# Kernel optimization log

Measured on AMD Instinct MI355X. Metric: run time of the kernel, lower is better.

## Reference

```python
import jax, jax.numpy as jnp
import numpy as np

EPS = 1e-06
H_BW = 0.5  # bandwidth h


def setup_inputs() -> dict:
    key = jax.random.key(0)
    k1, k2 = jax.random.split(key)
    N, C, H, W = 8, 256, 64, 64
    x = jax.random.normal(k1, (N, C, H, W), dtype=jnp.float32)
    y = jax.random.normal(k2, (N, C, H, W), dtype=jnp.float32)
    return {"x": x, "y": y}


def reference(x, y):
    N, C, _H, _W = x.shape
    # mean over W, H, then batch -> per-channel mean, shape (1, C, 1, 1)
    y_mu = y.mean(axis=3).mean(axis=2).mean(axis=0).reshape(1, C, 1, 1)
    x_c = x - y_mu
    y_c = y - y_mu
    # L2-normalize over channel dim (matches torch.norm without eps)
    x_n = x_c / jnp.linalg.norm(x_c, axis=1, keepdims=True)
    y_n = y_c / jnp.linalg.norm(y_c, axis=1, keepdims=True)
    x_n = x_n.reshape(N, C, -1)  # (N, C, HW)
    y_n = y_n.reshape(N, C, -1)
    # cosine similarity: (N, HW, HW)
    cosine_sim = jnp.einsum('nci,ncj->nij', x_n, y_n)
    d = 1.0 - cosine_sim
    d_min = jnp.min(d, axis=2, keepdims=True)
    d_tilde = d / (d_min + EPS)
    w = jnp.exp((1.0 - d_tilde) / H_BW)
    ccx_ij = w / jnp.sum(w, axis=2, keepdims=True)
    ccx = jnp.mean(jnp.max(ccx_ij, axis=1), axis=1)  # (N,)
    return jnp.mean(-jnp.log(ccx + EPS))
```

## Files before the change

### kernel.cpp

```cpp
#include <hip/hip_runtime.h>
#include <hip/hip_bf16.h>

#define HW 4096
#define CC 256
#define NBATCH 8
#define EPSF 1e-6f
#define SCL1 0x7F7F7F7F

typedef __attribute__((ext_vector_type(4))) float floatx4;
typedef __attribute__((ext_vector_type(8))) int intx8;
typedef long long llong;

#define GLDS(g, l) __builtin_amdgcn_global_load_lds( \
    (const __attribute__((address_space(1))) void*)(const void*)(g), \
    (__attribute__((address_space(3))) void*)(void*)(l), 16, 0, 0)

__device__ __forceinline__ unsigned fkey(float f){
    unsigned u = __float_as_uint(f);
    return (u & 0x80000000u) ? ~u : (u | 0x80000000u);
}
__device__ __forceinline__ float fdec(unsigned k){
    unsigned u = (k & 0x80000000u) ? (k ^ 0x80000000u) : ~k;
    return __uint_as_float(u);
}
__device__ __forceinline__ unsigned short f2bf(float f){
    unsigned u = __float_as_uint(f);
    u += 0x7FFFu + ((u >> 16) & 1);
    return (unsigned short)(u >> 16);
}

__global__ __launch_bounds__(256) void kmean(const float* __restrict__ y,
                                             float* __restrict__ ymu){
    const int c = blockIdx.x;
    const int t = threadIdx.x;
    float s = 0.f;
    for(int n = 0; n < NBATCH; n++){
        const float4* p = reinterpret_cast<const float4*>(y + ((size_t)n*CC + c)*HW);
        #pragma unroll
        for(int i = 0; i < 4; i++){
            float4 v = p[i*256 + t];
            s += (v.x + v.y) + (v.z + v.w);
        }
    }
    __shared__ float red[256];
    red[t] = s; __syncthreads();
    for(int off = 128; off > 0; off >>= 1){
        if(t < off) red[t] += red[t+off];
        __syncthreads();
    }
    if(t == 0) ymu[c] = red[0] * (1.0f/((float)NBATCH*HW));
}

#define TROW 264
__global__ __launch_bounds__(256) void knorm(const float* __restrict__ x,
                                             const float* __restrict__ y,
                                             const float* __restrict__ ymu,
                                             unsigned char* __restrict__ xF,
                                             unsigned char* __restrict__ yF,
                                             unsigned* __restrict__ dmink,
                                             float* __restrict__ rowsum,
                                             unsigned* __restrict__ colmaxk){
    __shared__ __align__(16) unsigned short tile[64*TROW];
    __shared__ float invn[64];
    __shared__ float partial[4][64];
    __shared__ float smu[CC];
    const int t   = threadIdx.x;
    const int hw0 = blockIdx.x * 64;
    const int n   = blockIdx.y;
    if(t < 64){
        size_t g = (size_t)n*HW + hw0 + t;
        dmink[g] = 0xFFFFFFFFu;
        rowsum[g] = 0.f;
        colmaxk[g] = 0u;
    }
    for(int c = t; c < CC; c += 256) smu[c] = ymu[c];
    const int hwl = t & 63;
    const int cch = t >> 6;
    for(int which = 0; which < 2; which++){
        const float* __restrict__ src = which ? y : x;
        unsigned char* __restrict__ dst = which ? yF : xF;
        __syncthreads();
        float ss = 0.f;
        for(int cc = 0; cc < 64; cc++){
            int c = cch*64 + cc;
            float v = src[((size_t)n*CC + c)*HW + hw0 + hwl] - smu[c];
            ss += v*v;
            tile[hwl*TROW + c] = f2bf(v);
        }
        partial[cch][hwl] = ss;
        __syncthreads();
        if(t < 64){
            float s = partial[0][t]+partial[1][t]+partial[2][t]+partial[3][t];
            invn[t] = rsqrtf(s);
        }
        __syncthreads();
        size_t base = ((size_t)n << 20) + (size_t)(hw0 >> 4)*4096;
        #pragma unroll
        for(int v4 = 0; v4 < 4; v4++){
            int g  = v4*256 + t;
            int it = g >> 8;
            int kt = (g >> 5) & 7;
            int qq = (g >> 3) & 3;
            int u  = g & 7;
            int r0 = it*16 + u*2;
            unsigned w[4];
            #pragma unroll
            for(int rr = 0; rr < 2; rr++){
                int r = r0 + rr;
                float inv = invn[r];
                const unsigned* lp = reinterpret_cast<const unsigned*>(&tile[r*TROW + kt*32 + qq*8]);
                float f[8];
                #pragma unroll
                for(int w2 = 0; w2 < 4; w2++){
                    unsigned uu = lp[w2];
                    f[2*w2]   = __uint_as_float((uu & 0xFFFFu) << 16) * inv;
                    f[2*w2+1] = __uint_as_float(uu & 0xFFFF0000u) * inv;
                }
                unsigned wa = 0, wb = 0;
                wa = __builtin_amdgcn_cvt_pk_fp8_f32(f[0], f[1], wa, false);
                wa = __builtin_amdgcn_cvt_pk_fp8_f32(f[2], f[3], wa, true);
                wb = __builtin_amdgcn_cvt_pk_fp8_f32(f[4], f[5], wb, false);
                wb = __builtin_amdgcn_cvt_pk_fp8_f32(f[6], f[7], wb, true);
                w[2*rr] = wa; w[2*rr+1] = wb;
            }
            uint4 ov; ov.x=w[0]; ov.y=w[1]; ov.z=w[2]; ov.w=w[3];
            *reinterpret_cast<uint4*>(dst + base + it*4096 + kt*512 + qq*128 + u*16) = ov;
        }
    }
}

union U8 { intx8 v; llong d[4]; };

template<int MODE>
__global__ __launch_bounds__(256, 2) void ksweep(
        const unsigned char* __restrict__ xF,
        const unsigned char* __restrict__ yF,
        unsigned* __restrict__ dmink,
        float* __restrict__ rowsum,
        unsigned* __restrict__ colmaxk){
    __shared__ __align__(16) unsigned char Bs[2][16384];
    __shared__ __align__(16) float scS[4][128];
    __shared__ __align__(16) float bbS[4][128];
    const int t    = threadIdx.x;
    const int lane = t & 63;
    const int wave = t >> 6;
    const int q    = lane >> 4;
    const int l15  = lane & 15;
    const int bid  = blockIdx.x;
    const int n    = bid & 7;
    const int rem  = bid >> 3;
    const int ip   = rem & 7;
    const int jq   = rem >> 3;
    const size_t nb8 = (size_t)n << 20;
    const size_t nbw = (size_t)n * HW;
    const int iw   = ip*512 + wave*128;
    const unsigned char* Ax = xF + nb8 + (size_t)(iw >> 4)*4096 + q*512 + l15*8;
    const unsigned char* Yb = yF + nb8 + (size_t)jq*131072;

    U8 af0[8], af1[8];
    #pragma unroll
    for(int ti = 0; ti < 8; ti++)
        #pragma unroll
        for(int qq = 0; qq < 4; qq++){
            af0[ti].d[qq] = *reinterpret_cast<const llong*>(Ax + ti*4096 + qq*128);
            af1[ti].d[qq] = *reinterpret_cast<const llong*>(Ax + ti*4096 + 2048 + qq*128);
        }

    if(MODE >= 1){
        #pragma unroll
        for(int rr = 0; rr < 2; rr++){
            int row = lane*2 + rr;
            size_t g = nbw + iw + row;
            scS[wave][row] = 2.f / (fdec(dmink[g]) + EPSF);
            if(MODE == 2) bbS[wave][row] = 2.f - __logf(rowsum[g]);
        }
    }
    float racc[8][4];
    #pragma unroll
    for(int ti = 0; ti < 8; ti++)
        #pragma unroll
        for(int r = 0; r < 4; r++) racc[ti][r] = (MODE == 0) ? -3e38f : 0.f;

    #pragma unroll
    for(int p = 0; p < 4; p++){
        int c = wave*4 + p;
        GLDS(Yb + c*1024 + (size_t)lane*16, &Bs[0][c*1024]);
    }
    __syncthreads();

    #pragma unroll 1
    for(int ss = 0; ss < 8; ss++){
        {
            const unsigned char* src = Yb + (size_t)(ss+1)*16384;
            unsigned char* dstb = Bs[(ss+1)&1];
            #pragma unroll
            for(int p = 0; p < 4; p++){
                int c = wave*4 + p;
                GLDS(src + c*1024 + (size_t)lane*16, &dstb[c*1024]);
            }
        }
        #pragma unroll 1
        for(int u = 0; u < 4; u++){
            const unsigned char* Bq = &Bs[ss&1][u*4096] + q*512 + l15*8;
            const int js = ss*4 + u;
            U8 b0, b1;
            #pragma unroll
            for(int qq = 0; qq < 4; qq++){
                b0.d[qq] = *reinterpret_cast<const llong*>(Bq + qq*128);
                b1.d[qq] = *reinterpret_cast<const llong*>(Bq + 2048 + qq*128);
            }
            floatx4 acc[8];
            #pragma unroll
            for(int a = 0; a < 8; a++) acc[a] = (floatx4){0.f,0.f,0.f,0.f};
            #pragma unroll
            for(int ti = 0; ti < 8; ti++){
                acc[ti] = __builtin_amdgcn_mfma_scale_f32_16x16x128_f8f6f4(
                              af0[ti].v, b0.v, acc[ti], 0, 0, 0, SCL1, 0, SCL1);
                acc[ti] = __builtin_amdgcn_mfma_scale_f32_16x16x128_f8f6f4(
                              af1[ti].v, b1.v, acc[ti], 0, 0, 0, SCL1, 0, SCL1);
            }
            if(MODE == 0){
                #pragma unroll
                for(int ti = 0; ti < 8; ti++)
                    #pragma unroll
                    for(int r = 0; r < 4; r++)
                        racc[ti][r] = fmaxf(racc[ti][r], acc[ti][r]);
            } else if(MODE == 1){
                #pragma unroll
                for(int ti = 0; ti < 8; ti++){
                    const floatx4 sc4 = *reinterpret_cast<const floatx4*>(&scS[wave][ti*16 + q*4]);
                    #pragma unroll
                    for(int r = 0; r < 4; r++)
                        racc[ti][r] += __expf(fmaf(acc[ti][r] - 1.f, sc4[r], 2.f));
                }
            } else {
                float a = -3e38f;
                #pragma unroll
                for(int ti = 0; ti < 8; ti++){
                    const floatx4 sc4 = *reinterpret_cast<const floatx4*>(&scS[wave][ti*16 + q*4]);
                    const floatx4 bb4 = *reinterpret_cast<const floatx4*>(&bbS[wave][ti*16 + q*4]);
                    #pragma unroll
                    for(int r = 0; r < 4; r++)
                        a = fmaxf(a, fmaf(acc[ti][r] - 1.f, sc4[r], bb4[r]));
                }
                a = fmaxf(a, __shfl_xor(a, 16));
                a = fmaxf(a, __shfl_xor(a, 32));
                if(lane < 16)
                    atomicMax(&colmaxk[nbw + jq*512 + js*16 + l15], fkey(__expf(a)));
            }
        }
        __syncthreads();
    }

    if(MODE == 0){
        #pragma unroll
        for(int ti = 0; ti < 8; ti++)
            #pragma unroll
            for(int r = 0; r < 4; r++){
                float v = racc[ti][r];
                v = fmaxf(v, __shfl_xor(v, 1));
                v = fmaxf(v, __shfl_xor(v, 2));
                v = fmaxf(v, __shfl_xor(v, 4));
                v = fmaxf(v, __shfl_xor(v, 8));
                if(l15 == 0)
                    atomicMin(&dmink[nbw + iw + ti*16 + q*4 + r], fkey(1.f - v));
            }
    } else if(MODE == 1){
        #pragma unroll
        for(int ti = 0; ti < 8; ti++)
            #pragma unroll
            for(int r = 0; r < 4; r++){
                float v = racc[ti][r];
                v += __shfl_xor(v, 1);
                v += __shfl_xor(v, 2);
                v += __shfl_xor(v, 4);
                v += __shfl_xor(v, 8);
                if(l15 == 0)
                    atomicAdd(&rowsum[nbw + iw + ti*16 + q*4 + r], v);
            }
    }
}

__global__ __launch_bounds__(256) void kpart(const unsigned* __restrict__ colmaxk,
                                             float* __restrict__ part){
    __shared__ float red[256];
    const int t = threadIdx.x;
    const int n = blockIdx.x;
    float s = 0.f;
    for(int j = t; j < HW; j += 256) s += fdec(colmaxk[(size_t)n*HW + j]);
    red[t] = s; __syncthreads();
    for(int off = 128; off > 0; off >>= 1){
        if(t < off) red[t] += red[t+off];
        __syncthreads();
    }
    if(t == 0) part[n] = -logf(red[0]*(1.0f/HW) + EPSF);
}

__global__ __launch_bounds__(64) void kfin(const float* __restrict__ part,
                                           float* __restrict__ out){
    const int t = threadIdx.x;
    float v = (t < NBATCH) ? part[t] : 0.f;
    v += __shfl_xor(v, 1);
    v += __shfl_xor(v, 2);
    v += __shfl_xor(v, 4);
    if(t == 0) out[0] = v * (1.0f/NBATCH);
}

extern "C" void kernel_launch(void* const* d_in, const int* in_sizes, int n_in,
                              void* d_out, int out_size, void* d_ws, size_t ws_size,
                              hipStream_t stream){
    const float* x = (const float*)d_in[0];
    const float* y = (const float*)d_in[1];
    float* out = (float*)d_out;
    char* ws = (char*)d_ws;

    float* ymu = (float*)ws;
    size_t off = 1024;
    unsigned char* xF = (unsigned char*)(ws + off); off += (size_t)NBATCH << 20;
    unsigned char* yF = (unsigned char*)(ws + off); off += ((size_t)NBATCH << 20) + (512<<10);
    unsigned* dmink   = (unsigned*)(ws + off);      off += (size_t)NBATCH*HW*4;
    float* rowsum     = (float*)(ws + off);         off += (size_t)NBATCH*HW*4;
    unsigned* colmaxk = (unsigned*)(ws + off);      off += (size_t)NBATCH*HW*4;
    float* part       = (float*)(ws + off);         off += 64;

    kmean<<<dim3(CC), dim3(256), 0, stream>>>(y, ymu);
    knorm<<<dim3(HW/64, NBATCH), dim3(256), 0, stream>>>(x, y, ymu, xF, yF,
                                                         dmink, rowsum, colmaxk);
    ksweep<0><<<dim3(512), dim3(256), 0, stream>>>(xF, yF, dmink, rowsum, colmaxk);
    ksweep<1><<<dim3(512), dim3(256), 0, stream>>>(xF, yF, dmink, rowsum, colmaxk);
    ksweep<2><<<dim3(512), dim3(256), 0, stream>>>(xF, yF, dmink, rowsum, colmaxk);
    kpart<<<dim3(NBATCH), dim3(256), 0, stream>>>(colmaxk, part);
    kfin<<<dim3(1), dim3(64), 0, stream>>>(part, out);
}
```

Baseline: 233.3 us.

## Vectorize norm loads, double-buffer B fragments, use exp2 and MFMA priority

The normalization kernel now reads x/y with float4 loads over a 16-channel-group layout, using a wider partial-sum array and a padded tile row stride to cut strided scalar global loads and LDS bank conflicts. The sweep kernel fully unrolls the inner u loop and prefetches the next B fragment from LDS into a second register slot while the current MFMAs run. It also raises wave priority around the MFMA block. The exp/log scaling is folded into base-2 constants so exp2f/log2f replace __expf/__logf. The cost is more registers, which could hurt occupancy at the 2-blocks-per-CU bound.

```diff
diff --git a/kernel.cpp b/kernel.cpp
--- a/kernel.cpp
+++ b/kernel.cpp
@@ -6,10 +6,14 @@
 #define NBATCH 8
 #define EPSF 1e-6f
 #define SCL1 0x7F7F7F7F
+#define LOG2E 1.44269504089f
+#define C2L   2.88539008177f
 
 typedef __attribute__((ext_vector_type(4))) float floatx4;
 typedef __attribute__((ext_vector_type(8))) int intx8;
 typedef long long llong;
+
+union U8 { intx8 v; llong d[4]; };
 
 #define GLDS(g, l) __builtin_amdgcn_global_load_lds( \
     (const __attribute__((address_space(1))) void*)(const void*)(g), \
@@ -51,7 +55,7 @@
     if(t == 0) ymu[c] = red[0] * (1.0f/((float)NBATCH*HW));
 }
 
-#define TROW 264
+#define TROW 266
 __global__ __launch_bounds__(256) void knorm(const float* __restrict__ x,
                                              const float* __restrict__ y,
                                              const float* __restrict__ ymu,
@@ -62,7 +66,7 @@
                                              unsigned* __restrict__ colmaxk){
     __shared__ __align__(16) unsigned short tile[64*TROW];
     __shared__ float invn[64];
-    __shared__ float partial[4][64];
+    __shared__ float partial16[16][64];
     __shared__ float smu[CC];
     const int t   = threadIdx.x;
     const int hw0 = blockIdx.x * 64;
@@ -74,30 +78,40 @@
         colmaxk[g] = 0u;
     }
     for(int c = t; c < CC; c += 256) smu[c] = ymu[c];
-    const int hwl = t & 63;
-    const int cch = t >> 6;
+    const int cgrp = t >> 4;
+    const int hwg  = t & 15;
     for(int which = 0; which < 2; which++){
         const float* __restrict__ src = which ? y : x;
         unsigned char* __restrict__ dst = which ? yF : xF;
         __syncthreads();
-        float ss = 0.f;
-        for(int cc = 0; cc < 64; cc++){
-            int c = cch*64 + cc;
-            float v = src[((size_t)n*CC + c)*HW + hw0 + hwl] - smu[c];
-            ss += v*v;
-            tile[hwl*TROW + c] = f2bf(v);
-        }
-        partial[cch][hwl] = ss;
+        float ss4[4] = {0.f, 0.f, 0.f, 0.f};
+        #pragma unroll
+        for(int cc = 0; cc < 16; cc++){
+            int c = cc*16 + cgrp;
+            float4 v4 = *reinterpret_cast<const float4*>(
+                &src[((size_t)n*CC + c)*HW + hw0 + hwg*4]);
+            float mu = smu[c];
+            float f0 = v4.x - mu, f1 = v4.y - mu, f2 = v4.z - mu, f3 = v4.w - mu;
+            ss4[0] += f0*f0; ss4[1] += f1*f1; ss4[2] += f2*f2; ss4[3] += f3*f3;
+            tile[(hwg*4+0)*TROW + c] = f2bf(f0);
+            tile[(hwg*4+1)*TROW + c] = f2bf(f1);
+            tile[(hwg*4+2)*TROW + c] = f2bf(f2);
+            tile[(hwg*4+3)*TROW + c] = f2bf(f3);
+        }
+        #pragma unroll
+        for(int e = 0; e < 4; e++) partial16[cgrp][hwg*4+e] = ss4[e];
         __syncthreads();
         if(t < 64){
-            float s = partial[0][t]+partial[1][t]+partial[2][t]+partial[3][t];
+            float s = 0.f;
+            #pragma unroll
+            for(int g2 = 0; g2 < 16; g2++) s += partial16[g2][t];
             invn[t] = rsqrtf(s);
         }
         __syncthreads();
         size_t base = ((size_t)n << 20) + (size_t)(hw0 >> 4)*4096;
         #pragma unroll
-        for(int v4 = 0; v4 < 4; v4++){
-            int g  = v4*256 + t;
+        for(int v4i = 0; v4i < 4; v4i++){
+            int g  = v4i*256 + t;
             int it = g >> 8;
             int kt = (g >> 5) & 7;
             int qq = (g >> 3) & 3;
@@ -128,8 +142,6 @@
         }
     }
 }
-
-union U8 { intx8 v; llong d[4]; };
 
 template<int MODE>
 __global__ __launch_bounds__(256, 2) void ksweep(
@@ -171,8 +183,8 @@
         for(int rr = 0; rr < 2; rr++){
             int row = lane*2 + rr;
             size_t g = nbw + iw + row;
-            scS[wave][row] = 2.f / (fdec(dmink[g]) + EPSF);
-            if(MODE == 2) bbS[wave][row] = 2.f - __logf(rowsum[g]);
+            scS[wave][row] = (2.f / (fdec(dmink[g]) + EPSF)) * LOG2E;
+            if(MODE == 2) bbS[wave][row] = C2L - __log2f(rowsum[g]);
         }
     }
     float racc[8][4];
@@ -180,6 +192,16 @@
     for(int ti = 0; ti < 8; ti++)
         #pragma unroll
         for(int r = 0; r < 4; r++) racc[ti][r] = (MODE == 0) ? -3e38f : 0.f;
+
+    U8 breg[2][2];
+    auto loadb = [&](int slot, const unsigned char* tilebase){
+        const unsigned char* Bq = tilebase + q*512 + l15*8;
+        #pragma unroll
+        for(int qq = 0; qq < 4; qq++){
+            breg[slot][0].d[qq] = *reinterpret_cast<const llong*>(Bq + qq*128);
+            breg[slot][1].d[qq] = *reinterpret_cast<const llong*>(Bq + 2048 + qq*128);
+        }
+    };
 
     #pragma unroll
     for(int p = 0; p < 4; p++){
@@ -190,6 +212,7 @@
 
     #pragma unroll 1
     for(int ss = 0; ss < 8; ss++){
+        loadb(0, &Bs[ss&1][0]);
         {
             const unsigned char* src = Yb + (size_t)(ss+1)*16384;
             unsigned char* dstb = Bs[(ss+1)&1];
@@ -199,19 +222,16 @@
                 GLDS(src + c*1024 + (size_t)lane*16, &dstb[c*1024]);
             }
         }
-        #pragma unroll 1
+        #pragma unroll
         for(int u = 0; u < 4; u++){
-            const unsigned char* Bq = &Bs[ss&1][u*4096] + q*512 + l15*8;
             const int js = ss*4 + u;
-            U8 b0, b1;
-            #pragma unroll
-            for(int qq = 0; qq < 4; qq++){
-                b0.d[qq] = *reinterpret_cast<const llong*>(Bq + qq*128);
-                b1.d[qq] = *reinterpret_cast<const llong*>(Bq + 2048 + qq*128);
-            }
+            if(u < 3) loadb((u+1)&1, &Bs[ss&1][(u+1)*4096]);
+            U8& b0 = breg[u&1][0];
+            U8& b1 = breg[u&1][1];
             floatx4 acc[8];
             #pragma unroll
             for(int a = 0; a < 8; a++) acc[a] = (floatx4){0.f,0.f,0.f,0.f};
+            __builtin_amdgcn_s_setprio(1);
             #pragma unroll
             for(int ti = 0; ti < 8; ti++){
                 acc[ti] = __builtin_amdgcn_mfma_scale_f32_16x16x128_f8f6f4(
@@ -219,6 +239,7 @@
                 acc[ti] = __builtin_amdgcn_mfma_scale_f32_16x16x128_f8f6f4(
                               af1[ti].v, b1.v, acc[ti], 0, 0, 0, SCL1, 0, SCL1);
             }
+            __builtin_amdgcn_s_setprio(0);
             if(MODE == 0){
                 #pragma unroll
                 for(int ti = 0; ti < 8; ti++)
@@ -231,7 +252,7 @@
                     const floatx4 sc4 = *reinterpret_cast<const floatx4*>(&scS[wave][ti*16 + q*4]);
                     #pragma unroll
                     for(int r = 0; r < 4; r++)
-                        racc[ti][r] += __expf(fmaf(acc[ti][r] - 1.f, sc4[r], 2.f));
+                        racc[ti][r] += exp2f(fmaf(acc[ti][r] - 1.f, sc4[r], C2L));
                 }
             } else {
                 float a = -3e38f;
@@ -246,7 +267,7 @@
                 a = fmaxf(a, __shfl_xor(a, 16));
                 a = fmaxf(a, __shfl_xor(a, 32));
                 if(lane < 16)
-                    atomicMax(&colmaxk[nbw + jq*512 + js*16 + l15], fkey(__expf(a)));
+                    atomicMax(&colmaxk[nbw + jq*512 + js*16 + l15], fkey(exp2f(a)));
             }
         }
         __syncthreads();
```

After: 298.1 us. 27.8% more time.
